# Kernel tuning notes

Hardware: AMD Instinct MI355X
Metric: run time of the kernel (lower is better)

## Reference

```python
import jax, jax.numpy as jnp
import numpy as np

N_NODES = 50000

def setup_inputs() -> dict:
    key = jax.random.key(0)
    k1, k2, k3, k4, k5 = jax.random.split(key, 5)
    x = jax.random.normal(k1, (50000, 512), dtype=jnp.float32)
    edge_row = jax.random.randint(k2, (800000,), 0, N_NODES, dtype=jnp.int64)
    edge_col = jax.random.randint(k3, (800000,), 0, N_NODES, dtype=jnp.int64)
    edge_val = jax.random.uniform(k4, (800000,), dtype=jnp.float32)
    # init like torch: uniform(-stdv, stdv), stdv = 1/sqrt(out_features)
    stdv = 1.0 / np.sqrt(96.0)
    weight = jax.random.uniform(k5, (512, 96), minval=-stdv, maxval=stdv, dtype=jnp.float32)
    return {"x": x, "edge_row": edge_row, "edge_col": edge_col, "edge_val": edge_val, "weight": weight}

def reference(x, edge_row, edge_col, edge_val, weight):
    # support = X @ W  -- dense GEMM [N, F_in] x [F_in, F_out]
    support = x @ weight
    # sparse adjacency matmul: out[row] += val * support[col]
    msgs = edge_val[:, None] * support[edge_col]          # [E, F_out]
    out = jax.ops.segment_sum(msgs, edge_row, num_segments=N_NODES)
    # act = ReLU (module default); bias=False
    return jax.nn.relu(out)
```

## Files before the change

### kernel.cpp

```cpp
#include <hip/hip_runtime.h>

#define N_NODES 50000
#define F_IN    512
#define F_OUT   96
#define N_EDGES 800000

#define RPB    128
#define NBKT   391
#define CAP    2560
#define ECHUNK 4096
#define NCHUNK ((N_EDGES + ECHUNK - 1) / ECHUNK)
#define GEMM_BLOCKS ((N_NODES + 63) / 64)

typedef __attribute__((ext_vector_type(8))) short bf16x8;
typedef __attribute__((ext_vector_type(4))) float f32x4;

typedef const __attribute__((address_space(1))) void* gas_ptr;
typedef __attribute__((address_space(3))) void* las_ptr;

__device__ __forceinline__ void gload_lds16(const void* g, void* l) {
    __builtin_amdgcn_global_load_lds((gas_ptr)g, (las_ptr)l, 16, 0, 0);
}

#define VMCNT_SB(n) do { \
    asm volatile("s_waitcnt vmcnt(" #n ")" ::: "memory"); \
    __builtin_amdgcn_sched_barrier(0); \
} while (0)

__device__ __forceinline__ unsigned short f2bf(float f) {
    unsigned int u = __float_as_uint(f);
    unsigned int r = (u + 0x7FFFu + ((u >> 16) & 1u)) >> 16;
    return (unsigned short)r;
}
__device__ __forceinline__ float bf2f(unsigned short h) {
    return __uint_as_float(((unsigned int)h) << 16);
}

__global__ __launch_bounds__(256) void k_wcast(const float* __restrict__ w,
                                               unsigned short* __restrict__ wTq,
                                               int* __restrict__ bcnt) {
    if (blockIdx.x == 0) {
        const int t = threadIdx.x;
        bcnt[t] = 0;
        if (t < 144) bcnt[256 + t] = 0;
    }
    const int i = blockIdx.x * 256 + threadIdx.x;
    if (i < F_OUT * F_IN) {
        const int j    = i & 7;
        const int lane = (i >> 3) & 63;
        const int ks   = (i >> 9) & 1;
        const int tp   = i >> 10;
        const int t    = tp % 6;
        const int p    = tp / 6;
        const int lr   = lane & 15;
        const int kg   = lane >> 4;
        const int n    = t * 16 + lr;
        const int k    = p * 64 + ks * 32 + kg * 8 + j;
        wTq[i] = f2bf(w[(size_t)k * F_OUT + n]);
    }
}

__global__ __launch_bounds__(256) void k_fused(const float* __restrict__ x,
                                               const unsigned short* __restrict__ wTq,
                                               unsigned short* __restrict__ support,
                                               const int* __restrict__ erow,
                                               const int* __restrict__ ecol,
                                               const float* __restrict__ eval,
                                               int* __restrict__ bcnt,
                                               float2* __restrict__ bucket) {
    __shared__ __align__(16) char smem[49152];
    const int tid = threadIdx.x;

    if (blockIdx.x < NCHUNK) {
        int* hist  = (int*)smem;
        int* gbase = hist + 400;
        int* lcur  = gbase + 400;
        for (int i = tid; i < NBKT; i += 256) { hist[i] = 0; lcur[i] = 0; }
        __syncthreads();

        const int base = blockIdx.x * ECHUNK;
        const int n = min(ECHUNK, N_EDGES - base);

        for (int i = tid; i < n; i += 256)
            atomicAdd(&hist[erow[base + i] >> 7], 1);
        __syncthreads();

        for (int b = tid; b < NBKT; b += 256)
            gbase[b] = hist[b] ? atomicAdd(&bcnt[b], hist[b]) : 0;
        __syncthreads();

        for (int i = tid; i < n; i += 256) {
            const int r = erow[base + i];
            const int b = r >> 7;
            const int pos = gbase[b] + atomicAdd(&lcur[b], 1);
            if (pos >= 0 && pos < CAP)
                bucket[(size_t)b * CAP + pos] = make_float2(
                    __int_as_float(((r & 127) << 16) | ecol[base + i]),
                    eval[base + i]);
        }
        return;
    }

    const int lane = tid & 63;
    const int wave = tid >> 6;
    const int r0   = (blockIdx.x - NCHUNK) * 64;
    const int lr   = lane & 15;
    const int kg   = lane >> 4;

    f32x4 acc[6];
    #pragma unroll
    for (int t = 0; t < 6; ++t) acc[t] = (f32x4){0.f, 0.f, 0.f, 0.f};

    auto STAGE = [&](int s, int p) {
        float* dst = (float*)(smem + s * 16384);
        #pragma unroll
        for (int i = 0; i < 4; ++i) {
            const int chunk = i * 256 + tid;
            const int row   = chunk >> 4;
            const int s16   = chunk & 15;
            int gr = r0 + row;
            if (gr > N_NODES - 1) gr = N_NODES - 1;
            const int srcb = (s16 * 16) ^ ((row & 15) << 4);
            gload_lds16(x + (size_t)gr * F_IN + p * 64 + (srcb >> 2),
                        dst + chunk * 4);
        }
    };
    auto COMPUTE = [&](int s, int p) {
        const float* xb = (const float*)(smem + s * 16384);
        const int xrow = wave * 16 + lr;
        const unsigned short* bbase = wTq + (size_t)p * 12 * 512 + lane * 8;
        #pragma unroll
        for (int ks = 0; ks < 2; ++ks) {
            const int byte0 = ks * 128 + kg * 32;
            const int b0 = byte0        ^ (lr << 4);
            const int b1 = (byte0 + 16) ^ (lr << 4);
            const float4 a0 = *reinterpret_cast<const float4*>(xb + xrow * 64 + (b0 >> 2));
            const float4 a1 = *reinterpret_cast<const float4*>(xb + xrow * 64 + (b1 >> 2));
            bf16x8 af;
            af[0] = (short)f2bf(a0.x); af[1] = (short)f2bf(a0.y);
            af[2] = (short)f2bf(a0.z); af[3] = (short)f2bf(a0.w);
            af[4] = (short)f2bf(a1.x); af[5] = (short)f2bf(a1.y);
            af[6] = (short)f2bf(a1.z); af[7] = (short)f2bf(a1.w);
            #pragma unroll
            for (int t = 0; t < 6; ++t) {
                const bf16x8 bq = *reinterpret_cast<const bf16x8*>(
                    bbase + (t * 2 + ks) * 512);
                acc[t] = __builtin_amdgcn_mfma_f32_16x16x32_bf16(af, bq, acc[t], 0, 0, 0);
            }
        }
    };

    STAGE(0, 0);
    STAGE(1, 1);

#define PANEL(p, vm) \
    do { \
        if ((p) + 2 < 8) STAGE(((p) + 2) % 3, (p) + 2); \
        VMCNT_SB(vm); \
        __builtin_amdgcn_s_barrier(); \
        COMPUTE((p) % 3, (p)); \
        __builtin_amdgcn_s_barrier(); \
    } while (0)

    PANEL(0, 8);
    PANEL(1, 8);
    PANEL(2, 8);
    PANEL(3, 8);
    PANEL(4, 8);
    PANEL(5, 8);
    PANEL(6, 4);
    PANEL(7, 0);
#undef PANEL

    #pragma unroll
    for (int t = 0; t < 6; ++t) {
        #pragma unroll
        for (int r = 0; r < 4; ++r) {
            const int row = r0 + wave * 16 + kg * 4 + r;
            if (row < N_NODES)
                support[(size_t)row * F_OUT + t * 16 + lr] = f2bf(acc[t][r]);
        }
    }
}

__global__ __launch_bounds__(256) void kS_sort(const int* __restrict__ bcnt,
                                               const float2* __restrict__ bucket,
                                               float2* __restrict__ bucket2,
                                               int* __restrict__ rowOffs) {
    __shared__ int cnt[RPB];
    __shared__ int sc[RPB];
    __shared__ int rbase[RPB];
    __shared__ int rcur[RPB];
    const int b   = blockIdx.x;
    const int tid = threadIdx.x;

    if (tid < RPB) { cnt[tid] = 0; rcur[tid] = 0; }
    __syncthreads();

    const int beg = b * CAP;
    const int n   = min(bcnt[b], CAP);

    for (int i = tid; i < n; i += 256)
        atomicAdd(&cnt[(__float_as_int(bucket[beg + i].x) >> 16) & 127], 1);
    __syncthreads();

    if (tid < RPB) sc[tid] = cnt[tid];
    __syncthreads();
    #pragma unroll
    for (int off = 1; off < RPB; off <<= 1) {
        int a = 0;
        if (tid < RPB && tid >= off) a = sc[tid - off];
        __syncthreads();
        if (tid < RPB) sc[tid] += a;
        __syncthreads();
    }
    if (tid < RPB) {
        const int rb = beg + sc[tid] - cnt[tid];
        rbase[tid] = rb;
        rowOffs[b * 129 + tid] = rb;
    }
    if (tid == RPB) rowOffs[b * 129 + RPB] = beg + n;
    __syncthreads();

    for (int i = tid; i < n; i += 256) {
        const float2 ev  = bucket[beg + i];
        const int    key = __float_as_int(ev.x);
        const int    r   = (key >> 16) & 127;
        const int    pos = rbase[r] + atomicAdd(&rcur[r], 1);
        bucket2[pos] = make_float2(__int_as_float(key & 0xFFFF), ev.y);
    }
}

__global__ __launch_bounds__(256) void k_gather(const int* __restrict__ rowOffs,
                                                const float2* __restrict__ bucket2,
                                                const unsigned short* __restrict__ support,
                                                float* __restrict__ out) {
    const int gid = blockIdx.x * 256 + threadIdx.x;
    if (gid >= N_NODES * 6) return;
    const int r   = gid / 6;
    const int f16 = gid - r * 6;

    const int idx = (r >> 7) * 129 + (r & 127);
    const int beg = rowOffs[idx];
    const int end = rowOffs[idx + 1];

    float acc[16];
    #pragma unroll
    for (int j = 0; j < 16; ++j) acc[j] = 0.f;

    for (int i = beg; i < end; ++i) {
        const float2 cv = bucket2[i];
        const int   c = __float_as_int(cv.x);
        const float v = cv.y;
        const unsigned short* sp = support + (size_t)c * F_OUT + f16 * 16;
        const bf16x8 s0 = *reinterpret_cast<const bf16x8*>(sp);
        const bf16x8 s1 = *reinterpret_cast<const bf16x8*>(sp + 8);
        #pragma unroll
        for (int j = 0; j < 8; ++j) {
            acc[j]     = fmaf(v, bf2f((unsigned short)s0[j]), acc[j]);
            acc[8 + j] = fmaf(v, bf2f((unsigned short)s1[j]), acc[8 + j]);
        }
    }

    float* o = out + (size_t)r * F_OUT + f16 * 16;
    #pragma unroll
    for (int q = 0; q < 4; ++q) {
        float4 ov;
        ov.x = fmaxf(acc[q * 4 + 0], 0.f);
        ov.y = fmaxf(acc[q * 4 + 1], 0.f);
        ov.z = fmaxf(acc[q * 4 + 2], 0.f);
        ov.w = fmaxf(acc[q * 4 + 3], 0.f);
        *reinterpret_cast<float4*>(o + q * 4) = ov;
    }
}

extern "C" void kernel_launch(void* const* d_in, const int* in_sizes, int n_in,
                              void* d_out, int out_size, void* d_ws, size_t ws_size,
                              hipStream_t stream) {
    const float* x    = (const float*)d_in[0];
    const int*   erow = (const int*)d_in[1];
    const int*   ecol = (const int*)d_in[2];
    const float* eval = (const float*)d_in[3];
    const float* w    = (const float*)d_in[4];
    float*       out  = (float*)d_out;

    unsigned short* support = (unsigned short*)d_ws;
    int*    bcnt    = (int*)((char*)d_ws + 9600000);
    int*    rowOffs = bcnt + 400;
    unsigned short* wTq = (unsigned short*)(rowOffs + 50560);
    float2* bucket  = (float2*)((char*)wTq + 98304);
    float2* bucket2 = bucket + (size_t)NBKT * CAP;

    k_wcast<<<(F_OUT * F_IN + 255) / 256, 256, 0, stream>>>(w, wTq, bcnt);

    k_fused<<<NCHUNK + GEMM_BLOCKS, 256, 0, stream>>>(x, wTq, support,
                                                      erow, ecol, eval,
                                                      bcnt, bucket);

    kS_sort<<<NBKT, 256, 0, stream>>>(bcnt, bucket, bucket2, rowOffs);

    const int gthreads = N_NODES * 6;
    k_gather<<<(gthreads + 255) / 256, 256, 0, stream>>>(rowOffs, bucket2, support, out);
}
```

Before: 83.12 us.

## Shrink GEMM row tile to 32 and issue all x loads upfront

The fused GEMM blocks now cover 32 rows instead of 64, and the four waves are arranged 2x2 over rows and output columns, each computing three 16-column tiles. Instead of a three-stage rolling pipeline, every block issues all sixteen async global-to-LDS loads for its full 32x512 x tile into 64KB of LDS at the start. Compute then steps through the panels, waiting on decreasing vmcnt values. This doubles the number of GEMM blocks for more parallelism and removes the mid-loop barriers, at the cost of higher LDS use per block (fewer resident blocks per CU) and more total reads of the weight matrix.

```diff
diff --git a/kernel.cpp b/kernel.cpp
--- a/kernel.cpp
+++ b/kernel.cpp
@@ -10,7 +10,8 @@
 #define CAP    2560
 #define ECHUNK 4096
 #define NCHUNK ((N_EDGES + ECHUNK - 1) / ECHUNK)
-#define GEMM_BLOCKS ((N_NODES + 63) / 64)
+#define BM     32
+#define GEMM_BLOCKS ((N_NODES + BM - 1) / BM)
 
 typedef __attribute__((ext_vector_type(8))) short bf16x8;
 typedef __attribute__((ext_vector_type(4))) float f32x4;
@@ -68,7 +69,7 @@
                                                const float* __restrict__ eval,
                                                int* __restrict__ bcnt,
                                                float2* __restrict__ bucket) {
-    __shared__ __align__(16) char smem[49152];
+    __shared__ __align__(16) char smem[65536];
     const int tid = threadIdx.x;
 
     if (blockIdx.x < NCHUNK) {
@@ -103,46 +104,47 @@
 
     const int lane = tid & 63;
     const int wave = tid >> 6;
-    const int r0   = (blockIdx.x - NCHUNK) * 64;
+    const int wr   = wave & 1;
+    const int wc   = wave >> 1;
+    const int r0   = (blockIdx.x - NCHUNK) * BM;
     const int lr   = lane & 15;
     const int kg   = lane >> 4;
 
-    f32x4 acc[6];
-    #pragma unroll
-    for (int t = 0; t < 6; ++t) acc[t] = (f32x4){0.f, 0.f, 0.f, 0.f};
-
-    auto STAGE = [&](int s, int p) {
-        float* dst = (float*)(smem + s * 16384);
-        #pragma unroll
-        for (int i = 0; i < 4; ++i) {
-            const int chunk = i * 256 + tid;
-            const int row   = chunk >> 4;
-            const int s16   = chunk & 15;
-            int gr = r0 + row;
-            if (gr > N_NODES - 1) gr = N_NODES - 1;
-            const int srcb = (s16 * 16) ^ ((row & 15) << 4);
-            gload_lds16(x + (size_t)gr * F_IN + p * 64 + (srcb >> 2),
-                        dst + chunk * 4);
-        }
-    };
-    auto COMPUTE = [&](int s, int p) {
-        const float* xb = (const float*)(smem + s * 16384);
-        const int xrow = wave * 16 + lr;
-        const unsigned short* bbase = wTq + (size_t)p * 12 * 512 + lane * 8;
+    f32x4 acc[3];
+    #pragma unroll
+    for (int t = 0; t < 3; ++t) acc[t] = (f32x4){0.f, 0.f, 0.f, 0.f};
+
+    #pragma unroll
+    for (int i = 0; i < 16; ++i) {
+        const int chunk = i * 256 + tid;
+        const int p     = chunk >> 9;
+        const int local = chunk & 511;
+        const int row   = local >> 4;
+        const int s16   = local & 15;
+        int gr = r0 + row;
+        if (gr > N_NODES - 1) gr = N_NODES - 1;
+        gload_lds16(x + (size_t)gr * F_IN + p * 64 + ((s16 ^ (row & 15)) << 2),
+                    smem + chunk * 16);
+    }
+
+    auto COMPUTE = [&](int p) {
+        const char* pb = smem + p * 8192;
+        const int row = wr * 16 + lr;
+        const unsigned short* bbase =
+            wTq + ((size_t)p * 12 + wc * 6) * 512 + lane * 8;
         #pragma unroll
         for (int ks = 0; ks < 2; ++ks) {
-            const int byte0 = ks * 128 + kg * 32;
-            const int b0 = byte0        ^ (lr << 4);
-            const int b1 = (byte0 + 16) ^ (lr << 4);
-            const float4 a0 = *reinterpret_cast<const float4*>(xb + xrow * 64 + (b0 >> 2));
-            const float4 a1 = *reinterpret_cast<const float4*>(xb + xrow * 64 + (b1 >> 2));
+            const int s0 = (ks * 8 + kg * 2)     ^ (row & 15);
+            const int s1 = (ks * 8 + kg * 2 + 1) ^ (row & 15);
+            const float4 a0 = *reinterpret_cast<const float4*>(pb + row * 256 + s0 * 16);
+            const float4 a1 = *reinterpret_cast<const float4*>(pb + row * 256 + s1 * 16);
             bf16x8 af;
             af[0] = (short)f2bf(a0.x); af[1] = (short)f2bf(a0.y);
             af[2] = (short)f2bf(a0.z); af[3] = (short)f2bf(a0.w);
             af[4] = (short)f2bf(a1.x); af[5] = (short)f2bf(a1.y);
             af[6] = (short)f2bf(a1.z); af[7] = (short)f2bf(a1.w);
             #pragma unroll
-            for (int t = 0; t < 6; ++t) {
+            for (int t = 0; t < 3; ++t) {
                 const bf16x8 bq = *reinterpret_cast<const bf16x8*>(
                     bbase + (t * 2 + ks) * 512);
                 acc[t] = __builtin_amdgcn_mfma_f32_16x16x32_bf16(af, bq, acc[t], 0, 0, 0);
@@ -150,35 +152,25 @@
         }
     };
 
-    STAGE(0, 0);
-    STAGE(1, 1);
-
 #define PANEL(p, vm) \
-    do { \
-        if ((p) + 2 < 8) STAGE(((p) + 2) % 3, (p) + 2); \
-        VMCNT_SB(vm); \
-        __builtin_amdgcn_s_barrier(); \
-        COMPUTE((p) % 3, (p)); \
-        __builtin_amdgcn_s_barrier(); \
-    } while (0)
-
-    PANEL(0, 8);
-    PANEL(1, 8);
-    PANEL(2, 8);
+    do { VMCNT_SB(vm); __builtin_amdgcn_s_barrier(); COMPUTE(p); } while (0)
+    PANEL(0, 14);
+    PANEL(1, 12);
+    PANEL(2, 10);
     PANEL(3, 8);
-    PANEL(4, 8);
-    PANEL(5, 8);
-    PANEL(6, 4);
+    PANEL(4, 6);
+    PANEL(5, 4);
+    PANEL(6, 2);
     PANEL(7, 0);
 #undef PANEL
 
     #pragma unroll
-    for (int t = 0; t < 6; ++t) {
+    for (int t = 0; t < 3; ++t) {
         #pragma unroll
         for (int r = 0; r < 4; ++r) {
-            const int row = r0 + wave * 16 + kg * 4 + r;
+            const int row = r0 + wr * 16 + kg * 4 + r;
             if (row < N_NODES)
-                support[(size_t)row * F_OUT + t * 16 + lr] = f2bf(acc[t][r]);
+                support[(size_t)row * F_OUT + wc * 48 + t * 16 + lr] = f2bf(acc[t][r]);
         }
     }
 }
```

Measured after the change: 88.80 us. 1.07x slower.
